# Performance work log

Hardware: AMD Instinct MI355X
Metric: run time of the kernel (lower is better)

Reference implementation:

```python
import jax, jax.numpy as jnp
import numpy as np

MASK_VAL = -1e30


def setup_inputs() -> dict:
    key = jax.random.key(0)
    ks = jax.random.split(key, 9)
    B, C, Q, D = 64, 2048, 128, 128
    s = 0.05  # small param init scale (xavier-like)
    return {
        "vfeats": jax.random.normal(ks[0], (B, C, D), jnp.float32),
        "qfeats": jax.random.normal(ks[1], (B, Q, D), jnp.float32),
        "vmask": jnp.ones((B, C), jnp.float32),
        "qmask": jnp.ones((B, Q), jnp.float32),
        "w4C": jax.random.normal(ks[2], (D, 1), jnp.float32) * s,
        "w4Q": jax.random.normal(ks[3], (D, 1), jnp.float32) * s,
        "w4mlu": jax.random.normal(ks[4], (1, 1, D), jnp.float32) * s,
        "cqa_W": jax.random.normal(ks[5], (D, 4 * D), jnp.float32) * s,  # Conv1D k=1 == Linear(4D->D)
        "cqa_b": jnp.zeros((D,), jnp.float32),
        "wp": jax.random.normal(ks[6], (D, 1), jnp.float32) * s,
        "cc_W": jax.random.normal(ks[7], (D, 2 * D), jnp.float32) * s,  # Conv1D k=1 == Linear(2D->D)
        "cc_b": jnp.zeros((D,), jnp.float32),
    }


def reference(vfeats, qfeats, vmask, qmask, w4C, w4Q, w4mlu, cqa_W, cqa_b, wp, cc_W, cc_b):
    # --- CQAttention ---
    # trilinear score: [B, C, Q]  (dropout is identity at inference)
    score = (vfeats @ w4C) \
        + jnp.swapaxes(qfeats @ w4Q, 1, 2) \
        + jnp.einsum('bcd,bqd->bcq', vfeats * w4mlu, qfeats)
    score_ = jax.nn.softmax(score + (1.0 - qmask[:, None, :]) * MASK_VAL, axis=2)   # [B,C,Q]
    score_t = jax.nn.softmax(score + (1.0 - vmask[:, :, None]) * MASK_VAL, axis=1)  # [B,C,Q]
    c2q = score_ @ qfeats                                                           # [B,C,D]
    # q2c = (score_ @ score_t^T) @ context; reassociate to avoid the [B,C,C] matrix
    q2c = score_ @ jnp.einsum('bcq,bcd->bqd', score_t, vfeats)                      # [B,C,D]
    cat = jnp.concatenate([vfeats, c2q, vfeats * c2q, vfeats * q2c], axis=2)        # [B,C,4D]
    feats = cat @ cqa_W.T + cqa_b                                                   # [B,C,D]
    # --- CQConcatenate (weighted pool of query) ---
    alpha = jax.nn.softmax((qfeats @ wp) + (1.0 - qmask[:, :, None]) * MASK_VAL, axis=1)  # [B,Q,1]
    pooled = jnp.einsum('bqd,bq->bd', qfeats, alpha[..., 0])                        # [B,D]
    pooled = jnp.broadcast_to(pooled[:, None, :], feats.shape)                      # [B,C,D]
    out = jnp.concatenate([feats, pooled], axis=2) @ cc_W.T + cc_b                  # [B,C,D]
    return jax.nn.relu(out)
```

## Files before the change

kernel.cpp:

```cpp
#include <hip/hip_runtime.h>
#include <stdint.h>

#define DI __device__ __forceinline__

typedef __attribute__((ext_vector_type(8))) short short8;
typedef __attribute__((ext_vector_type(4))) short short4v;
typedef __attribute__((ext_vector_type(4))) float float4v;

#define MFMA16(a, b, c) __builtin_amdgcn_mfma_f32_16x16x32_bf16((a), (b), (c), 0, 0, 0)

DI float b2f(short s) {
    uint32_t u = ((uint32_t)(uint16_t)s) << 16;
    float f;
    __builtin_memcpy(&f, &u, 4);
    return f;
}
DI short f2b(float f) {
    uint32_t x;
    __builtin_memcpy(&x, &f, 4);
    x += 0x7fffu + ((x >> 16) & 1u);
    return (short)(uint16_t)(x >> 16);
}


__global__ __launch_bounds__(256) void k_packfuse(const float* __restrict__ src, const float* __restrict__ wm,
                                                  const float* __restrict__ wv, const float* __restrict__ mask,
                                                  short* __restrict__ dstA, short* __restrict__ dstT,
                                                  float* __restrict__ dotout, int nkc) {
    __shared__ float St[32 * 133];
    int t = threadIdx.x, kc = blockIdx.x, b = blockIdx.y;
    int rl = t >> 3, sub = t & 7, dseg = sub * 16;
    int grow = (b * nkc + kc) * 32 + rl;
    const float* p = src + ((size_t)grow << 7) + dseg;
    float4v v[4];
#pragma unroll
    for (int g = 0; g < 4; ++g) v[g] = *(const float4v*)(p + g * 4);
    float s = 0.f;
#pragma unroll
    for (int g = 0; g < 4; ++g) {
        float4v wg = *(const float4v*)(wv + dseg + g * 4);
#pragma unroll
        for (int j = 0; j < 4; ++j) s += v[g][j] * wg[j];
    }
#pragma unroll
    for (int off = 1; off < 8; off <<= 1) s += __shfl_xor(s, off, 64);
    if (sub == 0) dotout[grow] = s + (1.f - mask[grow]) * (-1e30f);
#pragma unroll
    for (int g = 0; g < 4; ++g)
#pragma unroll
        for (int j = 0; j < 4; ++j) St[rl * 133 + dseg + g * 4 + j] = v[g][j];
#pragma unroll
    for (int h = 0; h < 2; ++h) {
        int c16 = sub * 2 + h;
        int ks = c16 >> 2, quad = c16 & 3;
        float4v m0 = wm ? *(const float4v*)(wm + c16 * 8) : (float4v){1.f, 1.f, 1.f, 1.f};
        float4v m1 = wm ? *(const float4v*)(wm + c16 * 8 + 4) : (float4v){1.f, 1.f, 1.f, 1.f};
        short8 o;
#pragma unroll
        for (int j = 0; j < 4; ++j) {
            o[j] = f2b(v[h * 2][j] * m0[j]);
            o[4 + j] = f2b(v[h * 2 + 1][j] * m1[j]);
        }
        int tile = b * (nkc * 2) + kc * 2 + (rl >> 4);
        *(short8*)(dstA + ((size_t)(tile * 4 + ks) << 9) + (quad * 16 + (rl & 15)) * 8) = o;
    }
    __syncthreads();
#pragma unroll
    for (int i = 0; i < 2; ++i) {
        int dt = (t >> 6) + i * 4;
        int lane = t & 63, ln = lane & 15, quad = lane >> 4;
        int d = dt * 16 + ln;
        short8 o;
#pragma unroll
        for (int j = 0; j < 8; ++j) o[j] = f2b(St[(quad * 8 + j) * 133 + d]);
        *(short8*)(dstT + (((size_t)(b * 8 + dt) * nkc + kc) << 9) + lane * 8) = o;
    }
}

__global__ __launch_bounds__(256) void k_packW(const float* __restrict__ wsrc, short* __restrict__ dst) {
    int idx = blockIdx.x * 256 + threadIdx.x;
    int lane = idx & 63, ks = (idx >> 6) & 3, part = (idx >> 8) & 3, nt = idx >> 10;
    const float* p = wsrc + (size_t)(nt * 16 + (lane & 15)) * 512 + part * 128 + ks * 32 + (lane >> 4) * 8;
    float4v a = *(const float4v*)p, b = *(const float4v*)(p + 4);
    short8 v;
#pragma unroll
    for (int j = 0; j < 4; ++j) {
        v[j] = f2b(a[j]);
        v[4 + j] = f2b(b[j]);
    }
    *(short8*)(dst + (size_t)idx * 8) = v;
}

__global__ __launch_bounds__(256) void k_packWc(const float* __restrict__ wsrc, short* __restrict__ dst) {
    int idx = blockIdx.x * 256 + threadIdx.x;
    int lane = idx & 63, ks = (idx >> 6) & 3, ot = idx >> 8;
    const float* p = wsrc + (size_t)(ot * 16 + (lane & 15)) * 256 + ks * 32 + (lane >> 4) * 8;
    float4v a = *(const float4v*)p, b = *(const float4v*)(p + 4);
    short8 v;
#pragma unroll
    for (int j = 0; j < 4; ++j) {
        v[j] = f2b(a[j]);
        v[4 + j] = f2b(b[j]);
    }
    *(short8*)(dst + (size_t)idx * 8) = v;
}

__global__ __launch_bounds__(128) void k_pool(const float* __restrict__ qf, const float* __restrict__ qmask,
                                              const float* __restrict__ wp, const float* __restrict__ ccW,
                                              const float* __restrict__ ccb, float* __restrict__ pc) {
    __shared__ float tmp[128], af[128], pooled[128];
    int b = blockIdx.x, t = threadIdx.x;
    const float* qrow = qf + ((size_t)(b * 128 + t) << 7);
    float s = 0.f;
    for (int d = 0; d < 128; ++d) s += qrow[d] * wp[d];
    s += (1.f - qmask[b * 128 + t]) * (-1e30f);
    tmp[t] = s;
    __syncthreads();
    for (int off = 64; off >= 1; off >>= 1) {
        if (t < off) tmp[t] = fmaxf(tmp[t], tmp[t + off]);
        __syncthreads();
    }
    float m = tmp[0];
    __syncthreads();
    float e = __expf(s - m);
    tmp[t] = e;
    __syncthreads();
    for (int off = 64; off >= 1; off >>= 1) {
        if (t < off) tmp[t] += tmp[t + off];
        __syncthreads();
    }
    af[t] = e / tmp[0];
    __syncthreads();
    float p = 0.f;
    for (int q = 0; q < 128; ++q) p += qf[((size_t)(b * 128 + q) << 7) + t] * af[q];
    pooled[t] = p;
    __syncthreads();
    float acc = ccb[t];
    for (int d = 0; d < 128; ++d) acc += pooled[d] * ccW[t * 256 + 128 + d];
    pc[b * 128 + t] = acc;
}

__global__ __launch_bounds__(256) void k_Tacc(const short* __restrict__ vfA, const short* __restrict__ vfT,
                                              const short* __restrict__ qfBW, const float* __restrict__ cvp,
                                              float* __restrict__ Pg, float* __restrict__ Csg) {
    __shared__ short Al[16 * 136];
    __shared__ float Red[4][16][130];
    __shared__ float csred[4][16];
    int tid = threadIdx.x, w = tid >> 6, lane = tid & 63, ln = lane & 15, quad = lane >> 4;
    int id = blockIdx.x;
    int xcd = id & 7, k = id >> 3;
    int g = xcd * 16 + (k & 15);
    int qt = k >> 4;
    int b = g & 63, s = g >> 6;
    short8 bq[4];
#pragma unroll
    for (int ks = 0; ks < 4; ++ks) bq[ks] = *(const short8*)(qfBW + (((size_t)(b * 8 + qt) * 4 + ks) << 9) + lane * 8);
    float4v acc[8];
#pragma unroll
    for (int dt = 0; dt < 8; ++dt) acc[dt] = (float4v){0.f, 0.f, 0.f, 0.f};
    float colacc = 0.f;
    for (int it = 0; it < 8; ++it) {
        int cbase = s * 1024 + it * 128 + w * 32;
        int ct = b * 128 + (cbase >> 4);
        float4v ds[2];
        ds[0] = (float4v){0.f, 0.f, 0.f, 0.f};
        ds[1] = (float4v){0.f, 0.f, 0.f, 0.f};
#pragma unroll
        for (int ks = 0; ks < 4; ++ks) {
#pragma unroll
            for (int mt = 0; mt < 2; ++mt) {
                short8 a = *(const short8*)(vfA + (((size_t)(ct + mt) * 4 + ks) << 9) + lane * 8);
                ds[mt] = MFMA16(a, bq[ks], ds[mt]);
            }
        }
#pragma unroll
        for (int mt = 0; mt < 2; ++mt) {
            float4v cv = *(const float4v*)(cvp + b * 2048 + cbase + mt * 16 + quad * 4);
            short4v ev;
#pragma unroll
            for (int r = 0; r < 4; ++r) {
                float e = __expf(ds[mt][r] + cv[r]);
                colacc += e;
                ev[r] = f2b(e);
            }
            *(short4v*)(Al + ln * 136 + w * 32 + mt * 16 + quad * 4) = ev;
        }
        short8 a = *(const short8*)(Al + ln * 136 + w * 32 + quad * 8);
#pragma unroll
        for (int dt = 0; dt < 8; ++dt) {
            short8 bb = *(const short8*)(vfT + (((size_t)(b * 8 + dt) * 64 + s * 32 + it * 4 + w) << 9) + lane * 8);
            acc[dt] = MFMA16(a, bb, acc[dt]);
        }
    }
#pragma unroll
    for (int dt = 0; dt < 8; ++dt)
#pragma unroll
        for (int r = 0; r < 4; ++r) Red[w][quad * 4 + r][dt * 16 + ln] = acc[dt][r];
    float p = colacc;
    p += __shfl_xor(p, 16, 64);
    p += __shfl_xor(p, 32, 64);
    if (lane < 16) csred[w][lane] = p;
    __syncthreads();
    if (tid < 16)
        Csg[((size_t)(s * 64 + b)) * 128 + qt * 16 + tid] =
            csred[0][tid] + csred[1][tid] + csred[2][tid] + csred[3][tid];
    {
        int q = tid >> 4, db = (tid & 15) * 8;
        float4v s0, s1;
#pragma unroll
        for (int j = 0; j < 4; ++j) {
            s0[j] = Red[0][q][db + j] + Red[1][q][db + j] + Red[2][q][db + j] + Red[3][q][db + j];
            s1[j] = Red[0][q][db + 4 + j] + Red[1][q][db + 4 + j] + Red[2][q][db + 4 + j] + Red[3][q][db + 4 + j];
        }
        size_t pb = (((size_t)(s * 64 + b)) * 8 + qt) * 2048 + q * 128 + db;
        *(float4v*)(Pg + pb) = s0;
        *(float4v*)(Pg + pb + 4) = s1;
    }
}

__global__ __launch_bounds__(256) void k_Tcomb(const float* __restrict__ Pg, const float* __restrict__ Csg,
                                               short* __restrict__ Ttf) {
    int idx = blockIdx.x * 256 + threadIdx.x;
    int lane = idx & 63, dt = (idx >> 8) & 7, b = idx >> 11;
    int d = dt * 16 + (lane & 15), q0 = ((idx >> 6) & 3) * 32 + (lane >> 4) * 8;
    short8 v;
#pragma unroll
    for (int j = 0; j < 8; ++j) {
        int q = q0 + j;
        size_t o0 = ((size_t)(b * 8) + (q >> 4)) * 2048 + (q & 15) * 128 + d;
        size_t o1 = ((size_t)((64 + b) * 8) + (q >> 4)) * 2048 + (q & 15) * 128 + d;
        float pv = Pg[o0] + Pg[o1];
        float cs = Csg[b * 128 + q] + Csg[(64 + b) * 128 + q];
        v[j] = f2b(pv / cs);
    }
    *(short8*)(Ttf + (size_t)idx * 8) = v;
}

__global__ __launch_bounds__(256, 4) void k_out(const short* __restrict__ vfA, const short* __restrict__ qfBW,
                                                const short* __restrict__ qTf, const short* __restrict__ Ttf,
                                                const float* __restrict__ qvp, const short* __restrict__ cqaWp,
                                                const float* __restrict__ cqab, const short* __restrict__ ccWp,
                                                const float* __restrict__ pc, float* __restrict__ out) {
    __shared__ short Sl[64 * 136];
    __shared__ short Xl[64 * 136];
    int tid = threadIdx.x, w = tid >> 6, lane = tid & 63, ln = lane & 15, quad = lane >> 4;
    int id = blockIdx.x;
    int xcd = id & 7, k = id >> 3;
    int b = xcd * 8 + (k & 7);
    int cx = k >> 3;
    int c0 = cx * 64 + w * 16;
    int tt = b * 128 + (c0 >> 4);
    int myrow = (w * 16 + ln) * 136;
    short8 av[4];
    {
        float4v sc[8];
#pragma unroll
        for (int qt = 0; qt < 8; ++qt) sc[qt] = (float4v){0.f, 0.f, 0.f, 0.f};
#pragma unroll
        for (int ks = 0; ks < 4; ++ks) {
            av[ks] = *(const short8*)(vfA + (((size_t)tt * 4 + ks) << 9) + lane * 8);
#pragma unroll
            for (int qt = 0; qt < 8; ++qt) {
                short8 bq = *(const short8*)(qfBW + (((size_t)(b * 8 + qt) * 4 + ks) << 9) + lane * 8);
                sc[qt] = MFMA16(av[ks], bq, sc[qt]);
            }
        }
        float qvl[8];
#pragma unroll
        for (int qt = 0; qt < 8; ++qt) qvl[qt] = qvp[b * 128 + qt * 16 + ln];
#pragma unroll
        for (int r = 0; r < 4; ++r) {
            float x[8], m = -3.4e38f;
#pragma unroll
            for (int qt = 0; qt < 8; ++qt) {
                x[qt] = sc[qt][r] + qvl[qt];
                m = fmaxf(m, x[qt]);
            }
#pragma unroll
            for (int off = 1; off < 16; off <<= 1) m = fmaxf(m, __shfl_xor(m, off, 64));
            float e[8], sm = 0.f;
#pragma unroll
            for (int qt = 0; qt < 8; ++qt) {
                e[qt] = __expf(x[qt] - m);
                sm += e[qt];
            }
#pragma unroll
            for (int off = 1; off < 16; off <<= 1) sm += __shfl_xor(sm, off, 64);
            float inv = 1.f / sm;
            int row = (w * 16 + quad * 4 + r) * 136;
#pragma unroll
            for (int qt = 0; qt < 8; ++qt) Sl[row + qt * 16 + ln] = f2b(e[qt] * inv);
        }
    }
    {
        float4v a2q[8];
#pragma unroll
        for (int dt = 0; dt < 8; ++dt) a2q[dt] = (float4v){0.f, 0.f, 0.f, 0.f};
#pragma unroll
        for (int ks = 0; ks < 4; ++ks) {
            short8 a = *(const short8*)(Sl + myrow + ks * 32 + quad * 8);
#pragma unroll
            for (int dt = 0; dt < 8; ++dt) {
                short8 b1 = *(const short8*)(qTf + (((size_t)(b * 8 + dt) * 4 + ks) << 9) + lane * 8);
                a2q[dt] = MFMA16(a, b1, a2q[dt]);
            }
        }
#pragma unroll
        for (int dt = 0; dt < 8; ++dt)
#pragma unroll
            for (int r = 0; r < 4; ++r) Xl[(w * 16 + quad * 4 + r) * 136 + dt * 16 + ln] = f2b(a2q[dt][r]);
    }
    {
        float4v aq2[8];
#pragma unroll
        for (int dt = 0; dt < 8; ++dt) aq2[dt] = (float4v){0.f, 0.f, 0.f, 0.f};
#pragma unroll
        for (int ks = 0; ks < 4; ++ks) {
            short8 a = *(const short8*)(Sl + myrow + ks * 32 + quad * 8);
#pragma unroll
            for (int dt = 0; dt < 8; ++dt) {
                short8 b2 = *(const short8*)(Ttf + (((size_t)(b * 8 + dt) * 4 + ks) << 9) + lane * 8);
                aq2[dt] = MFMA16(a, b2, aq2[dt]);
            }
        }
#pragma unroll
        for (int dt = 0; dt < 8; ++dt)
#pragma unroll
            for (int r = 0; r < 4; ++r) Sl[(w * 16 + quad * 4 + r) * 136 + dt * 16 + ln] = f2b(aq2[dt][r]);
    }
    float4v accF[8];
#pragma unroll
    for (int nt = 0; nt < 8; ++nt) accF[nt] = (float4v){0.f, 0.f, 0.f, 0.f};
#pragma unroll
    for (int ks = 0; ks < 4; ++ks) {
        short8 ac = *(const short8*)(Xl + myrow + ks * 32 + quad * 8);
        short8 aq = *(const short8*)(Sl + myrow + ks * 32 + quad * 8);
        short8 avc, avq;
#pragma unroll
        for (int j = 0; j < 8; ++j) {
            float fv = b2f(av[ks][j]);
            avc[j] = f2b(fv * b2f(ac[j]));
            avq[j] = f2b(fv * b2f(aq[j]));
        }
        short8 parts[4] = {av[ks], ac, avc, avq};
#pragma unroll
        for (int part = 0; part < 4; ++part) {
#pragma unroll
            for (int nt = 0; nt < 8; ++nt) {
                short8 bw = *(const short8*)(cqaWp + (((size_t)(nt * 4 + part) * 4 + ks) << 9) + lane * 8);
                accF[nt] = MFMA16(parts[part], bw, accF[nt]);
            }
        }
    }
#pragma unroll
    for (int nt = 0; nt < 8; ++nt) {
        int j = nt * 16 + ln;
        float bj = cqab[j];
#pragma unroll
        for (int r = 0; r < 4; ++r) Sl[(w * 16 + quad * 4 + r) * 136 + j] = f2b(accF[nt][r] + bj);
    }
    float4v accO[8];
#pragma unroll
    for (int ot = 0; ot < 8; ++ot) accO[ot] = (float4v){0.f, 0.f, 0.f, 0.f};
#pragma unroll
    for (int ks = 0; ks < 4; ++ks) {
        short8 a2 = *(const short8*)(Sl + myrow + ks * 32 + quad * 8);
#pragma unroll
        for (int ot = 0; ot < 8; ++ot) {
            short8 bw = *(const short8*)(ccWp + (((size_t)(ot * 4 + ks)) << 9) + lane * 8);
            accO[ot] = MFMA16(a2, bw, accO[ot]);
        }
    }
#pragma unroll
    for (int ot = 0; ot < 8; ++ot) {
        int o = ot * 16 + ln;
        float pco = pc[b * 128 + o];
#pragma unroll
        for (int r = 0; r < 4; ++r) {
            int c = c0 + quad * 4 + r;
            out[((size_t)(b * 2048 + c) << 7) + o] = fmaxf(accO[ot][r] + pco, 0.f);
        }
    }
}

extern "C" void kernel_launch(void* const* d_in, const int* in_sizes, int n_in, void* d_out, int out_size, void* d_ws,
                              size_t ws_size, hipStream_t stream) {
    const float* vf = (const float*)d_in[0];
    const float* qf = (const float*)d_in[1];
    const float* vmask = (const float*)d_in[2];
    const float* qmask = (const float*)d_in[3];
    const float* w4C = (const float*)d_in[4];
    const float* w4Q = (const float*)d_in[5];
    const float* w4mlu = (const float*)d_in[6];
    const float* cqaW = (const float*)d_in[7];
    const float* cqab = (const float*)d_in[8];
    const float* wp = (const float*)d_in[9];
    const float* ccW = (const float*)d_in[10];
    const float* ccb = (const float*)d_in[11];
    float* out = (float*)d_out;
    char* ws = (char*)d_ws;

    size_t o = 0;
    short* vfA = (short*)(ws + o); o += 64ull * 2048 * 128 * 2;
    short* vfT = (short*)(ws + o); o += 64ull * 2048 * 128 * 2;
    short* qfBW = (short*)(ws + o); o += 64ull * 128 * 128 * 2;
    short* qTf = (short*)(ws + o); o += 64ull * 128 * 128 * 2;
    short* Ttf = (short*)(ws + o); o += 64ull * 128 * 128 * 2;
    short* cqaWp = (short*)(ws + o); o += 128ull * 512 * 2;
    short* ccWp = (short*)(ws + o); o += 128ull * 128 * 2;
    float* Pg = (float*)(ws + o); o += 2ull * 64 * 128 * 128 * 4;
    float* Csg = (float*)(ws + o); o += 2ull * 64 * 128 * 4;
    float* cvp = (float*)(ws + o); o += 64ull * 2048 * 4;
    float* qvp = (float*)(ws + o); o += 64ull * 128 * 4;
    float* pc = (float*)(ws + o); o += 64ull * 128 * 4;

    k_packfuse<<<dim3(64, 64), 256, 0, stream>>>(vf, nullptr, w4C, vmask, vfA, vfT, cvp, 64);
    k_packfuse<<<dim3(4, 64), 256, 0, stream>>>(qf, w4mlu, w4Q, qmask, qfBW, qTf, qvp, 4);
    k_packW<<<32, 256, 0, stream>>>(cqaW, cqaWp);
    k_packWc<<<8, 256, 0, stream>>>(ccW, ccWp);
    k_pool<<<64, 128, 0, stream>>>(qf, qmask, wp, ccW, ccb, pc);
    k_Tacc<<<1024, 256, 0, stream>>>(vfA, vfT, qfBW, cvp, Pg, Csg);
    k_Tcomb<<<512, 256, 0, stream>>>(Pg, Csg, Ttf);
    k_out<<<2048, 256, 0, stream>>>(vfA, qfBW, qTf, Ttf, qvp, cqaWp, cqab, ccWp, pc, out);
}
```

Baseline: 280.1 us.

## Rewrite fused output kernel with 32x32 MFMA tiles and transposed orientation

Replaces the 16x16x32 MFMA output kernel with one that uses 32x32x16 bf16 MFMA, so each wave handles 32 context rows instead of 16 and the grid is halved. Computations are oriented so the context dimension maps to lanes, which lets the softmax row reduction use a single cross-half shuffle instead of a 16-lane butterfly. Intermediates are staged through a per-wave LDS scratch tile. This is meant to increase data reuse per B-fragment load and reduce shuffle and LDS work, at the cost of more registers (occupancy hint lowered to 3) and a more scattered output store pattern.

```diff
diff --git a/kernel.cpp b/kernel.cpp
--- a/kernel.cpp
+++ b/kernel.cpp
@@ -6,8 +6,10 @@
 typedef __attribute__((ext_vector_type(8))) short short8;
 typedef __attribute__((ext_vector_type(4))) short short4v;
 typedef __attribute__((ext_vector_type(4))) float float4v;
+typedef __attribute__((ext_vector_type(16))) float float16v;
 
 #define MFMA16(a, b, c) __builtin_amdgcn_mfma_f32_16x16x32_bf16((a), (b), (c), 0, 0, 0)
+#define MFMA32(a, b, c) __builtin_amdgcn_mfma_f32_32x32x16_bf16((a), (b), (c), 0, 0, 0)
 
 DI float b2f(short s) {
     uint32_t u = ((uint32_t)(uint16_t)s) << 16;
@@ -20,6 +22,13 @@
     __builtin_memcpy(&x, &f, 4);
     x += 0x7fffu + ((x >> 16) & 1u);
     return (short)(uint16_t)(x >> 16);
+}
+
+DI float16v zero16() {
+    float16v z;
+#pragma unroll
+    for (int i = 0; i < 16; ++i) z[i] = 0.f;
+    return z;
 }
 
 
@@ -236,151 +245,218 @@
     *(short8*)(Ttf + (size_t)idx * 8) = v;
 }
 
-__global__ __launch_bounds__(256, 4) void k_out(const short* __restrict__ vfA, const short* __restrict__ qfBW,
-                                                const short* __restrict__ qTf, const short* __restrict__ Ttf,
-                                                const float* __restrict__ qvp, const short* __restrict__ cqaWp,
-                                                const float* __restrict__ cqab, const short* __restrict__ ccWp,
-                                                const float* __restrict__ pc, float* __restrict__ out) {
-    __shared__ short Sl[64 * 136];
-    __shared__ short Xl[64 * 136];
-    int tid = threadIdx.x, w = tid >> 6, lane = tid & 63, ln = lane & 15, quad = lane >> 4;
+__global__ __launch_bounds__(256, 3) void k_out32(const short* __restrict__ vfA, const short* __restrict__ qfBW,
+                                                  const short* __restrict__ qTf, const short* __restrict__ Ttf,
+                                                  const float* __restrict__ qvp, const short* __restrict__ cqaWp,
+                                                  const float* __restrict__ cqab, const short* __restrict__ ccWp,
+                                                  const float* __restrict__ pc, float* __restrict__ out) {
+    __shared__ __align__(16) short Pl[4][32 * 132];
+    int tid = threadIdx.x, w = tid >> 6, l = tid & 63;
+    int h = l >> 5, c5 = l & 31, ln = c5 & 15, tadd = c5 >> 4;
     int id = blockIdx.x;
-    int xcd = id & 7, k = id >> 3;
-    int b = xcd * 8 + (k & 7);
-    int cx = k >> 3;
-    int c0 = cx * 64 + w * 16;
-    int tt = b * 128 + (c0 >> 4);
-    int myrow = (w * 16 + ln) * 136;
-    short8 av[4];
-    {
-        float4v sc[8];
-#pragma unroll
-        for (int qt = 0; qt < 8; ++qt) sc[qt] = (float4v){0.f, 0.f, 0.f, 0.f};
-#pragma unroll
-        for (int ks = 0; ks < 4; ++ks) {
-            av[ks] = *(const short8*)(vfA + (((size_t)tt * 4 + ks) << 9) + lane * 8);
-#pragma unroll
-            for (int qt = 0; qt < 8; ++qt) {
-                short8 bq = *(const short8*)(qfBW + (((size_t)(b * 8 + qt) * 4 + ks) << 9) + lane * 8);
-                sc[qt] = MFMA16(av[ks], bq, sc[qt]);
+    int xcd = id & 7, kk = id >> 3;
+    int b = xcd * 8 + (kk & 7);
+    int cblk = kk >> 3;
+    int ct2 = cblk * 4 + w;
+    int c0 = ct2 * 32;
+    short* myP = Pl[w];
+    int col = c5 * 132;
+    int loff0 = (h * 16 + ln) * 8;
+    int loff1 = ((2 + h) * 16 + ln) * 8;
+    int vbase = b * 128 + ct2 * 2 + tadd;
+
+#define FR32(p, t16, kc) \
+    (*(const short8*)((p) + (((size_t)(t16) * 4 + ((kc) >> 1)) << 9) + (((kc)&1) ? loff1 : loff0)))
+
+    float16v sc[4];
+#pragma unroll
+    for (int qt2 = 0; qt2 < 4; ++qt2) sc[qt2] = zero16();
+#pragma unroll
+    for (int kc = 0; kc < 8; ++kc) {
+        short8 bv = FR32(vfA, vbase, kc);
+#pragma unroll
+        for (int qt2 = 0; qt2 < 4; ++qt2) {
+            short8 aq = FR32(qfBW, b * 8 + qt2 * 2 + tadd, kc);
+            sc[qt2] = MFMA32(aq, bv, sc[qt2]);
+        }
+    }
+    float m = -3.4e38f;
+#pragma unroll
+    for (int qt2 = 0; qt2 < 4; ++qt2)
+#pragma unroll
+        for (int g = 0; g < 4; ++g) {
+            float4v qv = *(const float4v*)(qvp + b * 128 + qt2 * 32 + g * 8 + 4 * h);
+#pragma unroll
+            for (int r = 0; r < 4; ++r) {
+                float xv = sc[qt2][g * 4 + r] + qv[r];
+                sc[qt2][g * 4 + r] = xv;
+                m = fmaxf(m, xv);
             }
         }
-        float qvl[8];
-#pragma unroll
-        for (int qt = 0; qt < 8; ++qt) qvl[qt] = qvp[b * 128 + qt * 16 + ln];
-#pragma unroll
-        for (int r = 0; r < 4; ++r) {
-            float x[8], m = -3.4e38f;
-#pragma unroll
-            for (int qt = 0; qt < 8; ++qt) {
-                x[qt] = sc[qt][r] + qvl[qt];
-                m = fmaxf(m, x[qt]);
+    m = fmaxf(m, __shfl_xor(m, 32, 64));
+    float sm = 0.f;
+#pragma unroll
+    for (int qt2 = 0; qt2 < 4; ++qt2)
+#pragma unroll
+        for (int i = 0; i < 16; ++i) {
+            float e = __expf(sc[qt2][i] - m);
+            sc[qt2][i] = e;
+            sm += e;
+        }
+    sm += __shfl_xor(sm, 32, 64);
+    float inv = 1.f / sm;
+#pragma unroll
+    for (int qt2 = 0; qt2 < 4; ++qt2)
+#pragma unroll
+        for (int g = 0; g < 4; ++g) {
+            short4v o;
+#pragma unroll
+            for (int r = 0; r < 4; ++r) o[r] = f2b(sc[qt2][g * 4 + r] * inv);
+            *(short4v*)(myP + col + qt2 * 32 + g * 8 + 4 * h) = o;
+        }
+    short8 pb[8];
+#pragma unroll
+    for (int kc = 0; kc < 8; ++kc) {
+        short4v lo = *(const short4v*)(myP + col + kc * 16 + h * 8);
+        short4v hi = *(const short4v*)(myP + col + kc * 16 + h * 8 + 4);
+        short8 p8;
+#pragma unroll
+        for (int j = 0; j < 4; ++j) {
+            p8[j] = lo[j];
+            p8[4 + j] = hi[j];
+        }
+        pb[kc] = p8;
+    }
+    float16v cq[4];
+#pragma unroll
+    for (int dt2 = 0; dt2 < 4; ++dt2) cq[dt2] = zero16();
+#pragma unroll
+    for (int kc = 0; kc < 8; ++kc)
+#pragma unroll
+        for (int dt2 = 0; dt2 < 4; ++dt2) {
+            short8 a = FR32(qTf, b * 8 + dt2 * 2 + tadd, kc);
+            cq[dt2] = MFMA32(a, pb[kc], cq[dt2]);
+        }
+    short8 cb[8];
+#pragma unroll
+    for (int dt2 = 0; dt2 < 4; ++dt2)
+#pragma unroll
+        for (int g = 0; g < 4; ++g) {
+            short4v o;
+#pragma unroll
+            for (int r = 0; r < 4; ++r) o[r] = f2b(cq[dt2][g * 4 + r]);
+            *(short4v*)(myP + col + dt2 * 32 + g * 8 + 4 * h) = o;
+        }
+#pragma unroll
+    for (int kc = 0; kc < 8; ++kc) {
+        short4v lo = *(const short4v*)(myP + col + kc * 16 + h * 8);
+        short4v hi = *(const short4v*)(myP + col + kc * 16 + h * 8 + 4);
+        short8 p8;
+#pragma unroll
+        for (int j = 0; j < 4; ++j) {
+            p8[j] = lo[j];
+            p8[4 + j] = hi[j];
+        }
+        cb[kc] = p8;
+    }
+    float16v qc[4];
+#pragma unroll
+    for (int dt2 = 0; dt2 < 4; ++dt2) qc[dt2] = zero16();
+#pragma unroll
+    for (int kc = 0; kc < 8; ++kc)
+#pragma unroll
+        for (int dt2 = 0; dt2 < 4; ++dt2) {
+            short8 a = FR32(Ttf, b * 8 + dt2 * 2 + tadd, kc);
+            qc[dt2] = MFMA32(a, pb[kc], qc[dt2]);
+        }
+    short8 qb[8];
+#pragma unroll
+    for (int dt2 = 0; dt2 < 4; ++dt2)
+#pragma unroll
+        for (int g = 0; g < 4; ++g) {
+            short4v o;
+#pragma unroll
+            for (int r = 0; r < 4; ++r) o[r] = f2b(qc[dt2][g * 4 + r]);
+            *(short4v*)(myP + col + dt2 * 32 + g * 8 + 4 * h) = o;
+        }
+#pragma unroll
+    for (int kc = 0; kc < 8; ++kc) {
+        short4v lo = *(const short4v*)(myP + col + kc * 16 + h * 8);
+        short4v hi = *(const short4v*)(myP + col + kc * 16 + h * 8 + 4);
+        short8 p8;
+#pragma unroll
+        for (int j = 0; j < 4; ++j) {
+            p8[j] = lo[j];
+            p8[4 + j] = hi[j];
+        }
+        qb[kc] = p8;
+    }
+    float16v ft[4];
+#pragma unroll
+    for (int nt2 = 0; nt2 < 4; ++nt2) ft[nt2] = zero16();
+#pragma unroll
+    for (int kc = 0; kc < 8; ++kc) {
+        short8 vb = FR32(vfA, vbase, kc);
+        short8 pcb, pqb;
+#pragma unroll
+        for (int j = 0; j < 8; ++j) {
+            float fv = b2f(vb[j]);
+            pcb[j] = f2b(fv * b2f(cb[kc][j]));
+            pqb[j] = f2b(fv * b2f(qb[kc][j]));
+        }
+#pragma unroll
+        for (int part = 0; part < 4; ++part) {
+            short8 pB = (part == 0) ? vb : (part == 1) ? cb[kc] : (part == 2) ? pcb : pqb;
+#pragma unroll
+            for (int nt2 = 0; nt2 < 4; ++nt2) {
+                short8 aw = FR32(cqaWp, (nt2 * 2 + tadd) * 4 + part, kc);
+                ft[nt2] = MFMA32(aw, pB, ft[nt2]);
             }
-#pragma unroll
-            for (int off = 1; off < 16; off <<= 1) m = fmaxf(m, __shfl_xor(m, off, 64));
-            float e[8], sm = 0.f;
-#pragma unroll
-            for (int qt = 0; qt < 8; ++qt) {
-                e[qt] = __expf(x[qt] - m);
-                sm += e[qt];
-            }
-#pragma unroll
-            for (int off = 1; off < 16; off <<= 1) sm += __shfl_xor(sm, off, 64);
-            float inv = 1.f / sm;
-            int row = (w * 16 + quad * 4 + r) * 136;
-#pragma unroll
-            for (int qt = 0; qt < 8; ++qt) Sl[row + qt * 16 + ln] = f2b(e[qt] * inv);
-        }
-    }
-    {
-        float4v a2q[8];
-#pragma unroll
-        for (int dt = 0; dt < 8; ++dt) a2q[dt] = (float4v){0.f, 0.f, 0.f, 0.f};
-#pragma unroll
-        for (int ks = 0; ks < 4; ++ks) {
-            short8 a = *(const short8*)(Sl + myrow + ks * 32 + quad * 8);
-#pragma unroll
-            for (int dt = 0; dt < 8; ++dt) {
-                short8 b1 = *(const short8*)(qTf + (((size_t)(b * 8 + dt) * 4 + ks) << 9) + lane * 8);
-                a2q[dt] = MFMA16(a, b1, a2q[dt]);
-            }
-        }
-#pragma unroll
-        for (int dt = 0; dt < 8; ++dt)
-#pragma unroll
-            for (int r = 0; r < 4; ++r) Xl[(w * 16 + quad * 4 + r) * 136 + dt * 16 + ln] = f2b(a2q[dt][r]);
-    }
-    {
-        float4v aq2[8];
-#pragma unroll
-        for (int dt = 0; dt < 8; ++dt) aq2[dt] = (float4v){0.f, 0.f, 0.f, 0.f};
-#pragma unroll
-        for (int ks = 0; ks < 4; ++ks) {
-            short8 a = *(const short8*)(Sl + myrow + ks * 32 + quad * 8);
-#pragma unroll
-            for (int dt = 0; dt < 8; ++dt) {
-                short8 b2 = *(const short8*)(Ttf + (((size_t)(b * 8 + dt) * 4 + ks) << 9) + lane * 8);
-                aq2[dt] = MFMA16(a, b2, aq2[dt]);
-            }
-        }
-#pragma unroll
-        for (int dt = 0; dt < 8; ++dt)
-#pragma unroll
-            for (int r = 0; r < 4; ++r) Sl[(w * 16 + quad * 4 + r) * 136 + dt * 16 + ln] = f2b(aq2[dt][r]);
-    }
-    float4v accF[8];
-#pragma unroll
-    for (int nt = 0; nt < 8; ++nt) accF[nt] = (float4v){0.f, 0.f, 0.f, 0.f};
-#pragma unroll
-    for (int ks = 0; ks < 4; ++ks) {
-        short8 ac = *(const short8*)(Xl + myrow + ks * 32 + quad * 8);
-        short8 aq = *(const short8*)(Sl + myrow + ks * 32 + quad * 8);
-        short8 avc, avq;
-#pragma unroll
-        for (int j = 0; j < 8; ++j) {
-            float fv = b2f(av[ks][j]);
-            avc[j] = f2b(fv * b2f(ac[j]));
-            avq[j] = f2b(fv * b2f(aq[j]));
-        }
-        short8 parts[4] = {av[ks], ac, avc, avq};
-#pragma unroll
-        for (int part = 0; part < 4; ++part) {
-#pragma unroll
-            for (int nt = 0; nt < 8; ++nt) {
-                short8 bw = *(const short8*)(cqaWp + (((size_t)(nt * 4 + part) * 4 + ks) << 9) + lane * 8);
-                accF[nt] = MFMA16(parts[part], bw, accF[nt]);
-            }
-        }
-    }
-#pragma unroll
-    for (int nt = 0; nt < 8; ++nt) {
-        int j = nt * 16 + ln;
-        float bj = cqab[j];
-#pragma unroll
-        for (int r = 0; r < 4; ++r) Sl[(w * 16 + quad * 4 + r) * 136 + j] = f2b(accF[nt][r] + bj);
-    }
-    float4v accO[8];
-#pragma unroll
-    for (int ot = 0; ot < 8; ++ot) accO[ot] = (float4v){0.f, 0.f, 0.f, 0.f};
-#pragma unroll
-    for (int ks = 0; ks < 4; ++ks) {
-        short8 a2 = *(const short8*)(Sl + myrow + ks * 32 + quad * 8);
-#pragma unroll
-        for (int ot = 0; ot < 8; ++ot) {
-            short8 bw = *(const short8*)(ccWp + (((size_t)(ot * 4 + ks)) << 9) + lane * 8);
-            accO[ot] = MFMA16(a2, bw, accO[ot]);
-        }
-    }
-#pragma unroll
-    for (int ot = 0; ot < 8; ++ot) {
-        int o = ot * 16 + ln;
-        float pco = pc[b * 128 + o];
-#pragma unroll
-        for (int r = 0; r < 4; ++r) {
-            int c = c0 + quad * 4 + r;
-            out[((size_t)(b * 2048 + c) << 7) + o] = fmaxf(accO[ot][r] + pco, 0.f);
-        }
-    }
+        }
+    }
+#pragma unroll
+    for (int nt2 = 0; nt2 < 4; ++nt2)
+#pragma unroll
+        for (int g = 0; g < 4; ++g) {
+            float4v bj = *(const float4v*)(cqab + nt2 * 32 + g * 8 + 4 * h);
+            short4v o;
+#pragma unroll
+            for (int r = 0; r < 4; ++r) o[r] = f2b(ft[nt2][g * 4 + r] + bj[r]);
+            *(short4v*)(myP + col + nt2 * 32 + g * 8 + 4 * h) = o;
+        }
+    short8 fa[8];
+#pragma unroll
+    for (int kc = 0; kc < 8; ++kc) {
+        short4v lo = *(const short4v*)(myP + col + kc * 16 + h * 8);
+        short4v hi = *(const short4v*)(myP + col + kc * 16 + h * 8 + 4);
+        short8 p8;
+#pragma unroll
+        for (int j = 0; j < 4; ++j) {
+            p8[j] = lo[j];
+            p8[4 + j] = hi[j];
+        }
+        fa[kc] = p8;
+    }
+    float16v ao[4];
+#pragma unroll
+    for (int ot2 = 0; ot2 < 4; ++ot2) ao[ot2] = zero16();
+#pragma unroll
+    for (int kc = 0; kc < 8; ++kc)
+#pragma unroll
+        for (int ot2 = 0; ot2 < 4; ++ot2) {
+            short8 bw = FR32(ccWp, ot2 * 2 + tadd, kc);
+            ao[ot2] = MFMA32(fa[kc], bw, ao[ot2]);
+        }
+#pragma unroll
+    for (int ot2 = 0; ot2 < 4; ++ot2) {
+        float pco = pc[b * 128 + ot2 * 32 + c5];
+#pragma unroll
+        for (int i = 0; i < 16; ++i) {
+            int c = c0 + (i & 3) + 8 * (i >> 2) + 4 * h;
+            out[((size_t)(b * 2048 + c) << 7) + ot2 * 32 + c5] = fmaxf(ao[ot2][i] + pco, 0.f);
+        }
+    }
+#undef FR32
 }
 
 extern "C" void kernel_launch(void* const* d_in, const int* in_sizes, int n_in, void* d_out, int out_size, void* d_ws,
@@ -421,5 +497,5 @@
     k_pool<<<64, 128, 0, stream>>>(qf, qmask, wp, ccW, ccb, pc);
     k_Tacc<<<1024, 256, 0, stream>>>(vfA, vfT, qfBW, cvp, Pg, Csg);
     k_Tcomb<<<512, 256, 0, stream>>>(Pg, Csg, Ttf);
-    k_out<<<2048, 256, 0, stream>>>(vfA, qfBW, qTf, Ttf, qvp, cqaWp, cqab, ccWp, pc, out);
-}
+    k_out32<<<1024, 256, 0, stream>>>(vfA, qfBW, qTf, Ttf, qvp, cqaWp, cqab, ccWp, pc, out);
+}
```

Measured after the change: 343.7 us. +22.7%, slower.

## Split output GEMMs across waves by output columns instead of rows

Applied to the files above, without the earlier changes.

In the k_out kernel, the two projection GEMMs (cqa and cc) now have each wave compute all 64 rows of the block for 32 output columns, rather than its own 16 rows for all 128 columns. Each weight fragment loaded from global memory is reused across four row tiles, so per-wave weight traffic drops about fourfold. The cost is extra __syncthreads barriers, more shared-memory reads of the activation tiles, and the vfeats fragments for all rows being reloaded from global memory inside the loop.

```diff
diff --git a/kernel.cpp b/kernel.cpp
--- a/kernel.cpp
+++ b/kernel.cpp
@@ -251,18 +251,17 @@
     int c0 = cx * 64 + w * 16;
     int tt = b * 128 + (c0 >> 4);
     int myrow = (w * 16 + ln) * 136;
-    short8 av[4];
     {
         float4v sc[8];
 #pragma unroll
         for (int qt = 0; qt < 8; ++qt) sc[qt] = (float4v){0.f, 0.f, 0.f, 0.f};
 #pragma unroll
         for (int ks = 0; ks < 4; ++ks) {
-            av[ks] = *(const short8*)(vfA + (((size_t)tt * 4 + ks) << 9) + lane * 8);
+            short8 av = *(const short8*)(vfA + (((size_t)tt * 4 + ks) << 9) + lane * 8);
 #pragma unroll
             for (int qt = 0; qt < 8; ++qt) {
                 short8 bq = *(const short8*)(qfBW + (((size_t)(b * 8 + qt) * 4 + ks) << 9) + lane * 8);
-                sc[qt] = MFMA16(av[ks], bq, sc[qt]);
+                sc[qt] = MFMA16(av, bq, sc[qt]);
             }
         }
         float qvl[8];
@@ -328,59 +327,83 @@
 #pragma unroll
             for (int r = 0; r < 4; ++r) Sl[(w * 16 + quad * 4 + r) * 136 + dt * 16 + ln] = f2b(aq2[dt][r]);
     }
-    float4v accF[8];
-#pragma unroll
-    for (int nt = 0; nt < 8; ++nt) accF[nt] = (float4v){0.f, 0.f, 0.f, 0.f};
+    __syncthreads();
+    float4v accF[4][2];
+#pragma unroll
+    for (int ct = 0; ct < 4; ++ct)
+#pragma unroll
+        for (int nt2 = 0; nt2 < 2; ++nt2) accF[ct][nt2] = (float4v){0.f, 0.f, 0.f, 0.f};
 #pragma unroll
     for (int ks = 0; ks < 4; ++ks) {
-        short8 ac = *(const short8*)(Xl + myrow + ks * 32 + quad * 8);
-        short8 aq = *(const short8*)(Sl + myrow + ks * 32 + quad * 8);
-        short8 avc, avq;
-#pragma unroll
-        for (int j = 0; j < 8; ++j) {
-            float fv = b2f(av[ks][j]);
-            avc[j] = f2b(fv * b2f(ac[j]));
-            avq[j] = f2b(fv * b2f(aq[j]));
-        }
-        short8 parts[4] = {av[ks], ac, avc, avq};
+        short8 avk[4];
+#pragma unroll
+        for (int ct = 0; ct < 4; ++ct)
+            avk[ct] = *(const short8*)(vfA + (((size_t)(b * 128 + cx * 4 + ct) * 4 + ks) << 9) + lane * 8);
 #pragma unroll
         for (int part = 0; part < 4; ++part) {
-#pragma unroll
-            for (int nt = 0; nt < 8; ++nt) {
-                short8 bw = *(const short8*)(cqaWp + (((size_t)(nt * 4 + part) * 4 + ks) << 9) + lane * 8);
-                accF[nt] = MFMA16(parts[part], bw, accF[nt]);
-            }
-        }
-    }
-#pragma unroll
-    for (int nt = 0; nt < 8; ++nt) {
-        int j = nt * 16 + ln;
-        float bj = cqab[j];
-#pragma unroll
-        for (int r = 0; r < 4; ++r) Sl[(w * 16 + quad * 4 + r) * 136 + j] = f2b(accF[nt][r] + bj);
-    }
-    float4v accO[8];
-#pragma unroll
-    for (int ot = 0; ot < 8; ++ot) accO[ot] = (float4v){0.f, 0.f, 0.f, 0.f};
+            short8 a[4];
+#pragma unroll
+            for (int ct = 0; ct < 4; ++ct) {
+                int rowo = (ct * 16 + ln) * 136 + ks * 32 + quad * 8;
+                if (part == 0) {
+                    a[ct] = avk[ct];
+                } else if (part == 1) {
+                    a[ct] = *(const short8*)(Xl + rowo);
+                } else {
+                    short8 mfr = (part == 2) ? *(const short8*)(Xl + rowo) : *(const short8*)(Sl + rowo);
+#pragma unroll
+                    for (int j = 0; j < 8; ++j) a[ct][j] = f2b(b2f(avk[ct][j]) * b2f(mfr[j]));
+                }
+            }
+#pragma unroll
+            for (int nt2 = 0; nt2 < 2; ++nt2) {
+                short8 bw =
+                    *(const short8*)(cqaWp + (((size_t)((w * 2 + nt2) * 4 + part) * 4 + ks) << 9) + lane * 8);
+#pragma unroll
+                for (int ct = 0; ct < 4; ++ct) accF[ct][nt2] = MFMA16(a[ct], bw, accF[ct][nt2]);
+            }
+        }
+    }
+    __syncthreads();
+#pragma unroll
+    for (int ct = 0; ct < 4; ++ct)
+#pragma unroll
+        for (int nt2 = 0; nt2 < 2; ++nt2) {
+            int j = (w * 2 + nt2) * 16 + ln;
+            float bj = cqab[j];
+#pragma unroll
+            for (int r = 0; r < 4; ++r) Sl[(ct * 16 + quad * 4 + r) * 136 + j] = f2b(accF[ct][nt2][r] + bj);
+        }
+    __syncthreads();
+    float4v accO[4][2];
+#pragma unroll
+    for (int ct = 0; ct < 4; ++ct)
+#pragma unroll
+        for (int ot2 = 0; ot2 < 2; ++ot2) accO[ct][ot2] = (float4v){0.f, 0.f, 0.f, 0.f};
 #pragma unroll
     for (int ks = 0; ks < 4; ++ks) {
-        short8 a2 = *(const short8*)(Sl + myrow + ks * 32 + quad * 8);
-#pragma unroll
-        for (int ot = 0; ot < 8; ++ot) {
-            short8 bw = *(const short8*)(ccWp + (((size_t)(ot * 4 + ks)) << 9) + lane * 8);
-            accO[ot] = MFMA16(a2, bw, accO[ot]);
-        }
-    }
-#pragma unroll
-    for (int ot = 0; ot < 8; ++ot) {
-        int o = ot * 16 + ln;
-        float pco = pc[b * 128 + o];
-#pragma unroll
-        for (int r = 0; r < 4; ++r) {
-            int c = c0 + quad * 4 + r;
-            out[((size_t)(b * 2048 + c) << 7) + o] = fmaxf(accO[ot][r] + pco, 0.f);
-        }
-    }
+        short8 a[4];
+#pragma unroll
+        for (int ct = 0; ct < 4; ++ct) a[ct] = *(const short8*)(Sl + (ct * 16 + ln) * 136 + ks * 32 + quad * 8);
+#pragma unroll
+        for (int ot2 = 0; ot2 < 2; ++ot2) {
+            short8 bw = *(const short8*)(ccWp + (((size_t)((w * 2 + ot2) * 4 + ks)) << 9) + lane * 8);
+#pragma unroll
+            for (int ct = 0; ct < 4; ++ct) accO[ct][ot2] = MFMA16(a[ct], bw, accO[ct][ot2]);
+        }
+    }
+#pragma unroll
+    for (int ct = 0; ct < 4; ++ct)
+#pragma unroll
+        for (int ot2 = 0; ot2 < 2; ++ot2) {
+            int o = (w * 2 + ot2) * 16 + ln;
+            float pco = pc[b * 128 + o];
+#pragma unroll
+            for (int r = 0; r < 4; ++r) {
+                int c = cx * 64 + ct * 16 + quad * 4 + r;
+                out[((size_t)(b * 2048 + c) << 7) + o] = fmaxf(accO[ct][ot2][r] + pco, 0.f);
+            }
+        }
 }
 
 extern "C" void kernel_launch(void* const* d_in, const int* in_sizes, int n_in, void* d_out, int out_size, void* d_ws,
```

New measurement: 264.5 us. -5.6%, faster.
